# Performance work log

Measured on AMD Instinct MI355X. Metric: run time of the kernel, lower is better.

The kernel has to match this reference:

```python
import jax, jax.numpy as jnp
import numpy as np

PN = 1  # replication pad width for num_connected=9
OFFSETS = [(-1, -1), (-1, 0), (-1, 1), (0, -1), (0, 0), (0, 1), (1, -1), (1, 0), (1, 1)]
K = len(OFFSETS)


def setup_inputs() -> dict:
    key = jax.random.key(0)
    k1, k2, k3, k4 = jax.random.split(key, 4)
    B, Cin, Cv = 8, 128, 128
    H, W, I = 64, 64, 2
    guide = jax.random.normal(k1, (B, Cin, H * I, W * I), dtype=jnp.float32)
    value = jax.random.normal(k2, (B, Cv, H, W), dtype=jnp.float32)
    w_conv = jax.random.normal(k3, (K, Cin), dtype=jnp.float32) * 0.05  # 1x1 conv weight
    b_conv = jax.random.normal(k4, (K,), dtype=jnp.float32) * 0.05
    return {"guide": guide, "value": value, "w_conv": w_conv, "b_conv": b_conv}


def _make_offsets(x):
    # x: [B, C, H, W] -> [B, C, K, H, W] of replication-padded shifted neighbors
    B, C, H, W = x.shape
    xp = jnp.pad(x, ((0, 0), (0, 0), (PN, PN), (PN, PN)), mode="edge")
    slices = [xp[:, :, PN + o0:PN + o0 + H, PN + o1:PN + o1 + W] for (o0, o1) in OFFSETS]
    return jnp.stack(slices, axis=2)


def reference(guide, value, w_conv, b_conv):
    B, C, H, W = value.shape
    H_out, W_out = guide.shape[2], guide.shape[3]
    I = H_out // H
    # 1x1 conv: [B,Cin,Ho,Wo] x [K,Cin] -> [B,K,Ho,Wo]
    att = jnp.einsum("bchw,kc->bkhw", guide, w_conv) + b_conv[None, :, None, None]
    # conv_res=True, guide channels (Cin) > K: residual_auto adds guide[:, :K]
    att = guide[:, :K] + att
    att = jax.nn.softmax(att, axis=1)
    att = att.reshape(B, K, H, I, W, I)
    xk = _make_offsets(value)  # [B, C, K, H, W]
    # fused gather-multiply-reduce over the connection dim K
    res = jnp.einsum("bckhw,bkhiwj->bchiwj", xk, att)
    return res.reshape(B, C, H_out, W_out)
```

## Files before the change

kernel.cpp:

```cpp
#include <hip/hip_runtime.h>

#define NB 8
#define CH 128
#define HV 64
#define WV 64
#define HO 128
#define WO 128
#define KK 9

__global__ __launch_bounds__(256)
void la_att(const float* __restrict__ guide,
            const float* __restrict__ wconv,
            const float* __restrict__ bconv,
            float* __restrict__ att)
{
    const int tid = threadIdx.x;
    const int p  = blockIdx.x * 256 + tid;
    const int wo = p & 127;
    const int ho = (p >> 7) & 127;
    const int b  = p >> 14;

    const float* gpix = guide + ((size_t)b * CH) * (HO * WO) + ho * WO + wo;

    float a[KK];
    #pragma unroll
    for (int k = 0; k < KK; ++k)
        a[k] = bconv[k];

    #pragma unroll
    for (int c = 0; c < KK; ++c) {
        float g = gpix[(size_t)c * (HO * WO)];
        #pragma unroll
        for (int k = 0; k < KK; ++k)
            a[k] += g * wconv[k * CH + c];
        a[c] += g;
    }

    #pragma unroll 8
    for (int c = KK; c < CH; ++c) {
        float g = gpix[(size_t)c * (HO * WO)];
        #pragma unroll
        for (int k = 0; k < KK; ++k)
            a[k] += g * wconv[k * CH + c];
    }

    float m = a[0];
    #pragma unroll
    for (int k = 1; k < KK; ++k) m = fmaxf(m, a[k]);
    float s = 0.f;
    #pragma unroll
    for (int k = 0; k < KK; ++k) { a[k] = __expf(a[k] - m); s += a[k]; }
    float r = 1.0f / s;

    float* apix = att + ((size_t)b * KK) * (HO * WO) + ho * WO + wo;
    #pragma unroll
    for (int k = 0; k < KK; ++k)
        apix[(size_t)k * (HO * WO)] = a[k] * r;
}

#define HS 190
__global__ __launch_bounds__(128, 4)
void la_gather(const float* __restrict__ value,
               const float* __restrict__ att,
               float* __restrict__ out)
{
    __shared__ float s_halo[2][8 * HS];

    const int tid = threadIdx.x;
    const int blk = blockIdx.x;
    const int wt = blk & 3;
    const int ht = (blk >> 2) & 7;
    const int cg = (blk >> 5) & 7;
    const int b  = blk >> 8;

    const int tlw = tid & 7;
    const int tho = tid >> 3;
    const int ho = ht * 16 + tho;
    const int wo = wt * 32 + tlw * 4;

    const float* apix = att + ((size_t)b * KK) * (HO * WO) + ho * WO + wo;
    float a0[KK], a1[KK], a2[KK], a3[KK];
    #pragma unroll
    for (int k = 0; k < KK; ++k) {
        float4 av = *(const float4*)(apix + (size_t)k * (HO * WO));
        a0[k] = av.x; a1[k] = av.y; a2[k] = av.z; a3[k] = av.w;
    }

    const int c0 = cg * 16;
    const int h0 = ht * 8 - 1;
    const int w0 = wt * 16 - 1;
    const float* vb = value + (size_t)b * CH * (HV * WV);

    auto stage = [&](int g, int bf) {
        const float* vc = vb + (size_t)(c0 + g * 8) * (HV * WV);
        for (int i = tid; i < 8 * 180; i += 128) {
            int cc = i / 180;
            int r  = i - cc * 180;
            int hr = r / 18;
            int wr = r - hr * 18;
            int hh = min(max(h0 + hr, 0), HV - 1);
            int ww = min(max(w0 + wr, 0), WV - 1);
            s_halo[bf][cc * HS + hr * 19 + wr] =
                vc[(size_t)cc * (HV * WV) + hh * WV + ww];
        }
    };

    stage(0, 0);

    const int lh = tho >> 1;
    const int lw = tlw * 2;
    float* ob = out + (((size_t)b * CH + c0) * HO + ho) * WO + wo;

    #pragma unroll
    for (int g = 0; g < 2; ++g) {
        __syncthreads();
        if (g == 0) stage(1, 1);
        const float* buf = s_halo[g];
        #pragma unroll
        for (int cc = 0; cc < 8; ++cc) {
            const float* hp = &buf[cc * HS + lh * 19 + lw];
            float v00 = hp[0],  v01 = hp[1],  v02 = hp[2],  v03 = hp[3];
            float v10 = hp[19], v11 = hp[20], v12 = hp[21], v13 = hp[22];
            float v20 = hp[38], v21 = hp[39], v22 = hp[40], v23 = hp[41];
            float r0 = v00*a0[0] + v01*a0[1] + v02*a0[2]
                     + v10*a0[3] + v11*a0[4] + v12*a0[5]
                     + v20*a0[6] + v21*a0[7] + v22*a0[8];
            float r1 = v00*a1[0] + v01*a1[1] + v02*a1[2]
                     + v10*a1[3] + v11*a1[4] + v12*a1[5]
                     + v20*a1[6] + v21*a1[7] + v22*a1[8];
            float r2 = v01*a2[0] + v02*a2[1] + v03*a2[2]
                     + v11*a2[3] + v12*a2[4] + v13*a2[5]
                     + v21*a2[6] + v22*a2[7] + v23*a2[8];
            float r3 = v01*a3[0] + v02*a3[1] + v03*a3[2]
                     + v11*a3[3] + v12*a3[4] + v13*a3[5]
                     + v21*a3[6] + v22*a3[7] + v23*a3[8];
            float4 rr; rr.x = r0; rr.y = r1; rr.z = r2; rr.w = r3;
            *(float4*)(ob + (size_t)(g * 8 + cc) * (HO * WO)) = rr;
        }
    }
}

#define CCH 8
__global__ __launch_bounds__(128)
void la_fused(const float* __restrict__ guide,
              const float* __restrict__ value,
              const float* __restrict__ wconv,
              const float* __restrict__ bconv,
              float* __restrict__ out)
{
    __shared__ float s_wT[CH * 12];
    __shared__ float s_haloF[CCH * 110];

    const int tid = threadIdx.x;
    const int blk = blockIdx.x;
    const int wt = blk & 7;
    const int ht = (blk >> 3) & 7;
    const int b  = blk >> 6;

    for (int i = tid; i < KK * CH; i += 128) {
        int k = i >> 7;
        int c = i & 127;
        s_wT[c * 12 + k] = wconv[i];
    }

    const int tlwp = tid & 7;
    const int tho  = tid >> 3;
    const int ho = ht * 16 + tho;
    const int wo = wt * 16 + tlwp * 2;

    const float* gpix = guide + (((size_t)b * CH) * HO + ho) * WO + wo;

    float att0[KK], att1[KK];
    #pragma unroll
    for (int k = 0; k < KK; ++k) {
        float2 g = *(const float2*)(gpix + (size_t)k * (HO * WO));
        float bc = bconv[k];
        att0[k] = bc + g.x;
        att1[k] = bc + g.y;
    }
    __syncthreads();

    #pragma unroll 4
    for (int c = 0; c < CH; ++c) {
        float2 g = *(const float2*)(gpix + (size_t)c * (HO * WO));
        const float4* wt4 = (const float4*)&s_wT[c * 12];
        float4 wa = wt4[0];
        float4 wb = wt4[1];
        float w8 = s_wT[c * 12 + 8];
        att0[0] += g.x * wa.x;  att1[0] += g.y * wa.x;
        att0[1] += g.x * wa.y;  att1[1] += g.y * wa.y;
        att0[2] += g.x * wa.z;  att1[2] += g.y * wa.z;
        att0[3] += g.x * wa.w;  att1[3] += g.y * wa.w;
        att0[4] += g.x * wb.x;  att1[4] += g.y * wb.x;
        att0[5] += g.x * wb.y;  att1[5] += g.y * wb.y;
        att0[6] += g.x * wb.z;  att1[6] += g.y * wb.z;
        att0[7] += g.x * wb.w;  att1[7] += g.y * wb.w;
        att0[8] += g.x * w8;    att1[8] += g.y * w8;
    }

    float m0 = att0[0], m1 = att1[0];
    #pragma unroll
    for (int k = 1; k < KK; ++k) { m0 = fmaxf(m0, att0[k]); m1 = fmaxf(m1, att1[k]); }
    float s0 = 0.f, s1 = 0.f;
    #pragma unroll
    for (int k = 0; k < KK; ++k) {
        att0[k] = __expf(att0[k] - m0); s0 += att0[k];
        att1[k] = __expf(att1[k] - m1); s1 += att1[k];
    }
    float r0 = 1.0f / s0, r1 = 1.0f / s1;
    #pragma unroll
    for (int k = 0; k < KK; ++k) { att0[k] *= r0; att1[k] *= r1; }

    const int h0 = ht * 8 - 1;
    const int w0 = wt * 8 - 1;
    const int lh = tho >> 1;
    const float* vb = value + (size_t)b * CH * (HV * WV);
    float* ob = out + (((size_t)b * CH) * HO + ho) * WO + wo;

    for (int c0 = 0; c0 < CH; c0 += CCH) {
        __syncthreads();
        for (int i = tid; i < CCH * 100; i += 128) {
            int cc = i / 100;
            int r  = i - cc * 100;
            int hr = r / 10;
            int wr = r - hr * 10;
            int hh = min(max(h0 + hr, 0), HV - 1);
            int ww = min(max(w0 + wr, 0), WV - 1);
            s_haloF[cc * 110 + hr * 11 + wr] =
                vb[(size_t)(c0 + cc) * (HV * WV) + hh * WV + ww];
        }
        __syncthreads();
        #pragma unroll
        for (int cc = 0; cc < CCH; ++cc) {
            const float* hp = &s_haloF[cc * 110 + lh * 11 + tlwp];
            float v, q0, q1;
            v = hp[0];  q0  = v * att0[0]; q1  = v * att1[0];
            v = hp[1];  q0 += v * att0[1]; q1 += v * att1[1];
            v = hp[2];  q0 += v * att0[2]; q1 += v * att1[2];
            v = hp[11]; q0 += v * att0[3]; q1 += v * att1[3];
            v = hp[12]; q0 += v * att0[4]; q1 += v * att1[4];
            v = hp[13]; q0 += v * att0[5]; q1 += v * att1[5];
            v = hp[22]; q0 += v * att0[6]; q1 += v * att1[6];
            v = hp[23]; q0 += v * att0[7]; q1 += v * att1[7];
            v = hp[24]; q0 += v * att0[8]; q1 += v * att1[8];
            float2 rr; rr.x = q0; rr.y = q1;
            *(float2*)(ob + (size_t)(c0 + cc) * (HO * WO)) = rr;
        }
    }
}

extern "C" void kernel_launch(void* const* d_in, const int* in_sizes, int n_in,
                              void* d_out, int out_size, void* d_ws, size_t ws_size,
                              hipStream_t stream) {
    const float* guide = (const float*)d_in[0];
    const float* value = (const float*)d_in[1];
    const float* wconv = (const float*)d_in[2];
    const float* bconv = (const float*)d_in[3];
    float* outp = (float*)d_out;
    (void)in_sizes; (void)n_in; (void)out_size;

    const size_t att_bytes = (size_t)NB * KK * HO * WO * sizeof(float);
    if (ws_size >= att_bytes) {
        float* attp = (float*)d_ws;
        la_att<<<dim3(512), dim3(256), 0, stream>>>(guide, wconv, bconv, attp);
        la_gather<<<dim3(2048), dim3(128), 0, stream>>>(value, attp, outp);
    } else {
        la_fused<<<dim3(NB * 8 * 8), dim3(128), 0, stream>>>(guide, value, wconv, bconv, outp);
    }
}
```

Before: 155.4 us.

## Rewrite gather kernel with wavefront-per-row shuffles instead of LDS halo tiles

The gather kernel now assigns one 64-lane wavefront to each (batch, value row, 16-channel chunk). Each lane loads the three neighbouring value rows directly from global memory and gets its horizontal neighbours through lane shuffles. This removes the shared-memory halo staging, the double buffering and the block barriers, and relies on shuffle clamping at lanes 0 and 63 to reproduce edge replication. In exchange, each value row is loaded three times from global memory or cache, and the output store pattern changes to two float2 rows per lane.

```diff
diff --git a/kernel.cpp b/kernel.cpp
--- a/kernel.cpp
+++ b/kernel.cpp
@@ -58,85 +58,66 @@
         apix[(size_t)k * (HO * WO)] = a[k] * r;
 }
 
-#define HS 190
-__global__ __launch_bounds__(128, 4)
+#define CHUNK 16
+__global__ __launch_bounds__(256)
 void la_gather(const float* __restrict__ value,
                const float* __restrict__ att,
                float* __restrict__ out)
 {
-    __shared__ float s_halo[2][8 * HS];
-
-    const int tid = threadIdx.x;
-    const int blk = blockIdx.x;
-    const int wt = blk & 3;
-    const int ht = (blk >> 2) & 7;
-    const int cg = (blk >> 5) & 7;
-    const int b  = blk >> 8;
-
-    const int tlw = tid & 7;
-    const int tho = tid >> 3;
-    const int ho = ht * 16 + tho;
-    const int wo = wt * 32 + tlw * 4;
-
-    const float* apix = att + ((size_t)b * KK) * (HO * WO) + ho * WO + wo;
-    float a0[KK], a1[KK], a2[KK], a3[KK];
-    #pragma unroll
-    for (int k = 0; k < KK; ++k) {
-        float4 av = *(const float4*)(apix + (size_t)k * (HO * WO));
-        a0[k] = av.x; a1[k] = av.y; a2[k] = av.z; a3[k] = av.w;
-    }
-
-    const int c0 = cg * 16;
-    const int h0 = ht * 8 - 1;
-    const int w0 = wt * 16 - 1;
-    const float* vb = value + (size_t)b * CH * (HV * WV);
-
-    auto stage = [&](int g, int bf) {
-        const float* vc = vb + (size_t)(c0 + g * 8) * (HV * WV);
-        for (int i = tid; i < 8 * 180; i += 128) {
-            int cc = i / 180;
-            int r  = i - cc * 180;
-            int hr = r / 18;
-            int wr = r - hr * 18;
-            int hh = min(max(h0 + hr, 0), HV - 1);
-            int ww = min(max(w0 + wr, 0), WV - 1);
-            s_halo[bf][cc * HS + hr * 19 + wr] =
-                vc[(size_t)cc * (HV * WV) + hh * WV + ww];
+    const int tid   = threadIdx.x;
+    const int lane  = tid & 63;
+    const int wid   = blockIdx.x * 4 + (tid >> 6);
+    const int chunk = wid & 7;
+    const int h     = (wid >> 3) & 63;
+    const int b     = wid >> 9;
+
+    float a00[KK], a01[KK], a10[KK], a11[KK];
+    {
+        const float* ap = att + ((size_t)b * KK * HO + 2 * h) * WO + 2 * lane;
+        #pragma unroll
+        for (int k = 0; k < KK; ++k) {
+            float2 r0 = *(const float2*)(ap + (size_t)k * (HO * WO));
+            float2 r1 = *(const float2*)(ap + (size_t)k * (HO * WO) + WO);
+            a00[k] = r0.x; a01[k] = r0.y;
+            a10[k] = r1.x; a11[k] = r1.y;
         }
-    };
-
-    stage(0, 0);
-
-    const int lh = tho >> 1;
-    const int lw = tlw * 2;
-    float* ob = out + (((size_t)b * CH + c0) * HO + ho) * WO + wo;
-
-    #pragma unroll
-    for (int g = 0; g < 2; ++g) {
-        __syncthreads();
-        if (g == 0) stage(1, 1);
-        const float* buf = s_halo[g];
-        #pragma unroll
-        for (int cc = 0; cc < 8; ++cc) {
-            const float* hp = &buf[cc * HS + lh * 19 + lw];
-            float v00 = hp[0],  v01 = hp[1],  v02 = hp[2],  v03 = hp[3];
-            float v10 = hp[19], v11 = hp[20], v12 = hp[21], v13 = hp[22];
-            float v20 = hp[38], v21 = hp[39], v22 = hp[40], v23 = hp[41];
-            float r0 = v00*a0[0] + v01*a0[1] + v02*a0[2]
-                     + v10*a0[3] + v11*a0[4] + v12*a0[5]
-                     + v20*a0[6] + v21*a0[7] + v22*a0[8];
-            float r1 = v00*a1[0] + v01*a1[1] + v02*a1[2]
-                     + v10*a1[3] + v11*a1[4] + v12*a1[5]
-                     + v20*a1[6] + v21*a1[7] + v22*a1[8];
-            float r2 = v01*a2[0] + v02*a2[1] + v03*a2[2]
-                     + v11*a2[3] + v12*a2[4] + v13*a2[5]
-                     + v21*a2[6] + v22*a2[7] + v23*a2[8];
-            float r3 = v01*a3[0] + v02*a3[1] + v03*a3[2]
-                     + v11*a3[3] + v12*a3[4] + v13*a3[5]
-                     + v21*a3[6] + v22*a3[7] + v23*a3[8];
-            float4 rr; rr.x = r0; rr.y = r1; rr.z = r2; rr.w = r3;
-            *(float4*)(ob + (size_t)(g * 8 + cc) * (HO * WO)) = rr;
-        }
+    }
+
+    const int hm = (h > 0) ? h - 1 : 0;
+    const int hp = (h < HV - 1) ? h + 1 : HV - 1;
+    const float* vc  = value + ((size_t)b * CH + chunk * CHUNK) * (HV * WV) + lane;
+    const float* prm = vc + hm * WV;
+    const float* pr0 = vc + h  * WV;
+    const float* prp = vc + hp * WV;
+    float* ob = out + (((size_t)b * CH + chunk * CHUNK) * HO + 2 * h) * WO + 2 * lane;
+
+    #pragma unroll 4
+    for (int cc = 0; cc < CHUNK; ++cc) {
+        float vm = prm[(size_t)cc * (HV * WV)];
+        float v0 = pr0[(size_t)cc * (HV * WV)];
+        float vp = prp[(size_t)cc * (HV * WV)];
+        float vmL = __shfl_up(vm, 1), vmR = __shfl_down(vm, 1);
+        float v0L = __shfl_up(v0, 1), v0R = __shfl_down(v0, 1);
+        float vpL = __shfl_up(vp, 1), vpR = __shfl_down(vp, 1);
+
+        float s00 = vmL*a00[0] + vm*a00[1] + vmR*a00[2]
+                  + v0L*a00[3] + v0*a00[4] + v0R*a00[5]
+                  + vpL*a00[6] + vp*a00[7] + vpR*a00[8];
+        float s01 = vmL*a01[0] + vm*a01[1] + vmR*a01[2]
+                  + v0L*a01[3] + v0*a01[4] + v0R*a01[5]
+                  + vpL*a01[6] + vp*a01[7] + vpR*a01[8];
+        float s10 = vmL*a10[0] + vm*a10[1] + vmR*a10[2]
+                  + v0L*a10[3] + v0*a10[4] + v0R*a10[5]
+                  + vpL*a10[6] + vp*a10[7] + vpR*a10[8];
+        float s11 = vmL*a11[0] + vm*a11[1] + vmR*a11[2]
+                  + v0L*a11[3] + v0*a11[4] + v0R*a11[5]
+                  + vpL*a11[6] + vp*a11[7] + vpR*a11[8];
+
+        float* oc = ob + (size_t)cc * (HO * WO);
+        float2 r0; r0.x = s00; r0.y = s01;
+        float2 r1; r1.x = s10; r1.y = s11;
+        *(float2*)oc        = r0;
+        *(float2*)(oc + WO) = r1;
     }
 }
 
@@ -263,7 +244,7 @@
     if (ws_size >= att_bytes) {
         float* attp = (float*)d_ws;
         la_att<<<dim3(512), dim3(256), 0, stream>>>(guide, wconv, bconv, attp);
-        la_gather<<<dim3(2048), dim3(128), 0, stream>>>(value, attp, outp);
+        la_gather<<<dim3(1024), dim3(256), 0, stream>>>(value, attp, outp);
     } else {
         la_fused<<<dim3(NB * 8 * 8), dim3(128), 0, stream>>>(guide, value, wconv, bconv, outp);
     }
```

New measurement: 168.7 us. +8.6%, slower.
